# Performance work log

Measured on AMD Instinct MI355X. Metric: run time of the kernel, lower is better.

## Reference

```python
import jax, jax.numpy as jnp
import numpy as np

DIM = 192
NUM_HEADS = 8
EPS = 1e-12  # torch F.normalize default eps


def setup_inputs() -> dict:
    key = jax.random.key(0)
    k1, k2, k3, k4 = jax.random.split(key, 4)
    b, c, h, w = 8, DIM, 128, 128
    x = jax.random.normal(k1, (b, c, h, w), dtype=jnp.float32)
    # 1x1 qkv conv weight, stored as (3c, c)
    w_qkv = jax.random.normal(k2, (3 * c, c), dtype=jnp.float32) * (1.0 / np.sqrt(c))
    # depthwise 3x3 conv weight, groups = 3c -> OIHW (3c, 1, 3, 3)
    w_dw = jax.random.normal(k3, (3 * c, 1, 3, 3), dtype=jnp.float32) * (1.0 / 3.0)
    # 1x1 project_out weight (c, c)
    w_out = jax.random.normal(k4, (c, c), dtype=jnp.float32) * (1.0 / np.sqrt(c))
    temperature = jnp.ones((NUM_HEADS, 1, 1), dtype=jnp.float32)
    return {"x": x, "w_qkv": w_qkv, "w_dw": w_dw, "w_out": w_out,
            "temperature": temperature}


def _mdta(x, w_qkv, w_dw, w_out, temperature):
    b, c, h, w = x.shape
    nh = NUM_HEADS
    # 1x1 conv == channel GEMM
    qkv = jnp.einsum('oc,bchw->bohw', w_qkv, x)
    # depthwise 3x3 conv, groups = 3c
    qkv = jax.lax.conv_general_dilated(
        qkv, w_dw, window_strides=(1, 1), padding='SAME',
        feature_group_count=3 * c,
        dimension_numbers=('NCHW', 'OIHW', 'NCHW'))
    q, k, v = jnp.split(qkv, 3, axis=1)
    hd = c // nh
    q = q.reshape(b, nh, hd, h * w)
    k = k.reshape(b, nh, hd, h * w)
    v = v.reshape(b, nh, hd, h * w)
    # L2 normalize over spatial (hw) dim
    q = q / jnp.maximum(jnp.linalg.norm(q, axis=-1, keepdims=True), EPS)
    k = k / jnp.maximum(jnp.linalg.norm(k, axis=-1, keepdims=True), EPS)
    # channel x channel attention per head: (b, nh, hd, hd)
    attn = jnp.einsum('bhcn,bhdn->bhcd', q, k) * temperature
    attn = jax.nn.softmax(attn, axis=-1)
    out = jnp.einsum('bhcd,bhdn->bhcn', attn, v).reshape(b, c, h, w)
    return jnp.einsum('oc,bchw->bohw', w_out, out)


def reference(x, w_qkv, w_dw, w_out, temperature):
    return _mdta(x, w_qkv, w_dw, w_out, temperature)
```

## Files before the change

### kernel.cpp

```cpp
#include <hip/hip_runtime.h>


#define HW 16384
#define WIMG 128
#define C 192
#define C3 576
#define NH 8
#define HD 24

typedef unsigned short ushort8_t __attribute__((ext_vector_type(8)));
typedef unsigned short ushort4_t __attribute__((ext_vector_type(4)));
typedef short short8_t __attribute__((ext_vector_type(8)));
typedef float float4_t __attribute__((ext_vector_type(4)));

__device__ __forceinline__ float bfu2f(unsigned short u) {
    union { unsigned int i; float f; } v; v.i = ((unsigned int)u) << 16; return v.f;
}
__device__ __forceinline__ unsigned short f2bfu(float f) {
    union { float f; unsigned int i; } v; v.f = f;
    unsigned int x = v.i;
    return (unsigned short)((x + 0x7FFFu + ((x >> 16) & 1u)) >> 16);
}
__device__ __forceinline__ float inload(const void* p, int idx, int isbf) {
    return isbf ? bfu2f(((const unsigned short*)p)[idx]) : ((const float*)p)[idx];
}

__global__ void probe_dtype(const unsigned int* __restrict__ x, int* __restrict__ flag) {
    const int t = threadIdx.x;
    int cnt = 0;
    for (int i = t; i < 512; i += 256) {
        const unsigned int u = x[i] & 0xFFFFu;
        const unsigned int e = (u >> 7) & 0xFFu;
        if (u == 0u || (e >= 100u && e <= 140u)) cnt++;
    }
#pragma unroll
    for (int off = 32; off; off >>= 1) cnt += __shfl_down(cnt, off, 64);
    __shared__ int s[4];
    if ((t & 63) == 0) s[t >> 6] = cnt;
    __syncthreads();
    if (t == 0) flag[0] = (s[0] + s[1] + s[2] + s[3] > 300) ? 1 : 0;
}

__global__ void prep(const void* __restrict__ wqkv, const void* __restrict__ wdw,
                     const void* __restrict__ wout, const void* __restrict__ temp,
                     const int* __restrict__ flagp, unsigned short* __restrict__ wqb,
                     float* __restrict__ wdwf, float* __restrict__ woutf,
                     float* __restrict__ tempf, float* __restrict__ Sraw,
                     float* __restrict__ normsum) {
    const int isbf = flagp[0];
    const int id = blockIdx.x * 256 + threadIdx.x;
    const int stride = gridDim.x * 256;
    for (int i = id; i < C3 * C; i += stride)
        wqb[i] = isbf ? ((const unsigned short*)wqkv)[i] : f2bfu(((const float*)wqkv)[i]);
    for (int i = id; i < C3 * 9; i += stride) wdwf[i] = inload(wdw, i, isbf);
    for (int i = id; i < C * C; i += stride) woutf[i] = inload(wout, i, isbf);
    for (int i = id; i < NH; i += stride) tempf[i] = inload(temp, i, isbf);
    for (int i = id; i < 8 * NH * HD * HD; i += stride) Sraw[i] = 0.f;
    for (int i = id; i < 8 * 2 * C; i += stride) normsum[i] = 0.f;
}

__global__ __launch_bounds__(512) void gemm_mfma(
    const void* __restrict__ Bsrc, const unsigned short* __restrict__ Abf,
    void* __restrict__ outp, const int* __restrict__ flagp,
    size_t b_batch_stride, size_t b_const_off, size_t o_batch_stride,
    int a_batch_stride, int m_tiles, int b_mode, int out_mode) {
    __shared__ unsigned short xT[24576];
    const int isbf = flagp[0];
    const int b_isbf = b_mode | isbf;
    const int tid = threadIdx.x;
    const int batch = blockIdx.y;
    const int n0 = blockIdx.x * 128;
    const size_t b_off = b_batch_stride * batch + b_const_off;
    const size_t o_off = o_batch_stride * batch;
    const unsigned short* Ab = Abf + (size_t)a_batch_stride * batch;

    if (tid < 384) {
        const int cg = tid >> 4;
        const int pg = tid & 15;
        ushort8_t rows[8];
        if (b_isbf) {
            const unsigned short* bp = (const unsigned short*)Bsrc + b_off + n0 + pg * 8;
#pragma unroll
            for (int r = 0; r < 8; r++)
                rows[r] = *reinterpret_cast<const ushort8_t*>(bp + (size_t)(cg * 8 + r) * HW);
        } else {
            const float* bp = (const float*)Bsrc + b_off + n0 + pg * 8;
#pragma unroll
            for (int r = 0; r < 8; r++) {
                const float4_t f0 = *reinterpret_cast<const float4_t*>(bp + (size_t)(cg * 8 + r) * HW);
                const float4_t f1 = *reinterpret_cast<const float4_t*>(bp + (size_t)(cg * 8 + r) * HW + 4);
#pragma unroll
                for (int i = 0; i < 4; i++) { rows[r][i] = f2bfu(f0[i]); rows[r][i + 4] = f2bfu(f1[i]); }
            }
        }
#pragma unroll
        for (int s = 0; s < 8; s++) {
            ushort8_t outv;
#pragma unroll
            for (int r = 0; r < 8; r++) outv[r] = rows[r][s];
            const int p = pg * 8 + s;
            const int cidx = p * 24 + (cg ^ (p & 7));
            *reinterpret_cast<ushort8_t*>(&xT[cidx * 8]) = outv;
        }
    }

    const int w = tid >> 6;
    const int lane = tid & 63;
    const int l15 = lane & 15;
    const int quad = lane >> 4;
    const int mhalf = w & 1;
    const int nquad = w >> 1;

    __syncthreads();

    short8_t bfr[6][2];
#pragma unroll
    for (int ks = 0; ks < 6; ks++)
#pragma unroll
        for (int nt = 0; nt < 2; nt++) {
            const int p = nquad * 32 + nt * 16 + l15;
            const int cg = ks * 4 + quad;
            const int cidx = p * 24 + (cg ^ (p & 7));
            bfr[ks][nt] = *reinterpret_cast<const short8_t*>(&xT[cidx * 8]);
        }

    const int o_isbf = out_mode ? isbf : 1;
    for (int mt0 = 0; mt0 < m_tiles; mt0++) {
        const int m0 = mt0 * 64;
        short8_t afr[2][6];
#pragma unroll
        for (int mt = 0; mt < 2; mt++) {
            const int row = m0 + (mhalf * 2 + mt) * 16 + l15;
#pragma unroll
            for (int ks = 0; ks < 6; ks++)
                afr[mt][ks] = *reinterpret_cast<const short8_t*>(Ab + (size_t)row * C + ks * 32 + quad * 8);
        }
        float4_t acc[2][2];
#pragma unroll
        for (int mt = 0; mt < 2; mt++)
#pragma unroll
            for (int nt = 0; nt < 2; nt++) {
                float4_t z = {0.f, 0.f, 0.f, 0.f};
                acc[mt][nt] = z;
            }
#pragma unroll
        for (int ks = 0; ks < 6; ks++)
#pragma unroll
            for (int mt = 0; mt < 2; mt++)
#pragma unroll
                for (int nt = 0; nt < 2; nt++)
                    acc[mt][nt] = __builtin_amdgcn_mfma_f32_16x16x32_bf16(
                        afr[mt][ks], bfr[ks][nt], acc[mt][nt], 0, 0, 0);
#pragma unroll
        for (int mt = 0; mt < 2; mt++) {
            const int row = m0 + (mhalf * 2 + mt) * 16 + quad * 4;
#pragma unroll
            for (int nt = 0; nt < 2; nt++) {
                const int col = n0 + nquad * 32 + nt * 16 + l15;
#pragma unroll
                for (int r = 0; r < 4; r++) {
                    const size_t idx = o_off + (size_t)(row + r) * HW + col;
                    if (o_isbf) ((unsigned short*)outp)[idx] = f2bfu(acc[mt][nt][r]);
                    else ((float*)outp)[idx] = acc[mt][nt][r];
                }
            }
        }
    }
}

__global__ void dwconv(const unsigned short* __restrict__ qkv0,
                       const float* __restrict__ wdwf,
                       unsigned short* __restrict__ qkv1,
                       float* __restrict__ normsum) {
    const int ch = blockIdx.y;
    const size_t base = (size_t)blockIdx.z * C3 * HW + (size_t)ch * HW;
    const unsigned short* ip = qkv0 + base;
    const float* wp = wdwf + ch * 9;
    const int p = blockIdx.x * 2048 + threadIdx.x * 8;
    const int y = p >> 7, x0 = p & 127;
    float acc[8];
#pragma unroll
    for (int j = 0; j < 8; j++) acc[j] = 0.f;
#pragma unroll
    for (int dy = 0; dy < 3; dy++) {
        const int yy = y + dy - 1;
        if (yy < 0 || yy > 127) continue;
        const int rb = yy * WIMG + x0;
        const ushort8_t mid = *reinterpret_cast<const ushort8_t*>(ip + rb);
        float f[10];
        f[0] = (x0 > 0) ? bfu2f(ip[rb - 1]) : 0.f;
        f[9] = (x0 < 120) ? bfu2f(ip[rb + 8]) : 0.f;
#pragma unroll
        for (int i = 0; i < 8; i++) f[i + 1] = bfu2f(mid[i]);
        const float w0 = wp[dy * 3], w1 = wp[dy * 3 + 1], w2 = wp[dy * 3 + 2];
#pragma unroll
        for (int j = 0; j < 8; j++) acc[j] += w0 * f[j] + w1 * f[j + 1] + w2 * f[j + 2];
    }
    ushort8_t outv;
#pragma unroll
    for (int j = 0; j < 8; j++) outv[j] = f2bfu(acc[j]);
    *reinterpret_cast<ushort8_t*>(qkv1 + base + p) = outv;

    if (ch < 2 * C) {
        float ss = 0.f;
#pragma unroll
        for (int j = 0; j < 8; j++) ss += acc[j] * acc[j];
#pragma unroll
        for (int off = 32; off; off >>= 1) ss += __shfl_down(ss, off, 64);
        __shared__ float red[4];
        if ((threadIdx.x & 63) == 0) red[threadIdx.x >> 6] = ss;
        __syncthreads();
        if (threadIdx.x == 0)
            atomicAdd(&normsum[blockIdx.z * 2 * C + ch],
                      red[0] + red[1] + red[2] + red[3]);
    }
}

__global__ __launch_bounds__(256) void attn_gram(
    const unsigned short* __restrict__ qkv1, float* __restrict__ Sraw) {
    const int b = blockIdx.z, h = blockIdx.y;
    const int wave = threadIdx.x >> 6;
    const int lane = threadIdx.x & 63;
    const int l15 = lane & 15, quad = lane >> 4;
    const int k0 = (blockIdx.x * 4 + wave) * 512;
    const unsigned short* qrow = qkv1 + (size_t)b * C3 * HW + (size_t)(h * HD) * HW;
    const unsigned short* krow = qkv1 + (size_t)b * C3 * HW + (size_t)(C + h * HD) * HW;

    float4_t acc[2][2];
#pragma unroll
    for (int mt = 0; mt < 2; mt++)
#pragma unroll
        for (int nt = 0; nt < 2; nt++) {
            float4_t z = {0.f, 0.f, 0.f, 0.f};
            acc[mt][nt] = z;
        }

#pragma unroll 4
    for (int ks = 0; ks < 16; ks++) {
        const int kk = k0 + ks * 32 + quad * 8;
        short8_t qa[2], kb[2];
        qa[0] = *reinterpret_cast<const short8_t*>(qrow + (size_t)l15 * HW + kk);
        qa[1] = *reinterpret_cast<const short8_t*>(qrow + (size_t)(16 + l15) * HW + kk);
        kb[0] = *reinterpret_cast<const short8_t*>(krow + (size_t)l15 * HW + kk);
        kb[1] = *reinterpret_cast<const short8_t*>(krow + (size_t)(16 + l15) * HW + kk);
#pragma unroll
        for (int mt = 0; mt < 2; mt++)
#pragma unroll
            for (int nt = 0; nt < 2; nt++)
                acc[mt][nt] = __builtin_amdgcn_mfma_f32_16x16x32_bf16(
                    qa[mt], kb[nt], acc[mt][nt], 0, 0, 0);
    }

    float* Sb = Sraw + (size_t)b * NH * HD * HD + (size_t)h * HD * HD;
#pragma unroll
    for (int nt = 0; nt < 2; nt++) {
        const int j = nt * 16 + l15;
        if (j >= HD) continue;
#pragma unroll
        for (int mt = 0; mt < 2; mt++) {
            const int i0 = mt * 16 + quad * 4;
#pragma unroll
            for (int r = 0; r < 4; r++) {
                const int i = i0 + r;
                if (i < HD) atomicAdd(&Sb[i * HD + j], acc[mt][nt][r]);
            }
        }
    }
}

__global__ void buildM(const float* __restrict__ Sraw, const float* __restrict__ normsum,
                       const float* __restrict__ tempf, const float* __restrict__ woutf,
                       unsigned short* __restrict__ Mb) {
    __shared__ float As[NH * HD * HD];
    __shared__ float inv[2 * C];
    const int b = blockIdx.y;
    const int tid = threadIdx.x;
    for (int r = tid; r < 2 * C; r += 256)
        inv[r] = 1.f / fmaxf(sqrtf(normsum[b * 2 * C + r]), 1e-12f);
    __syncthreads();
    for (int e = tid; e < NH * HD * HD; e += 256) {
        const int h = e / (HD * HD);
        const int rm = e - h * HD * HD;
        const int i = rm / HD, j = rm % HD;
        As[e] = Sraw[(size_t)b * NH * HD * HD + e] * inv[h * HD + i] * inv[C + h * HD + j] * tempf[h];
    }
    __syncthreads();
    if (tid < C) {
        const int h = tid / HD, i = tid % HD;
        float* rp = As + h * HD * HD + i * HD;
        float mx = -1e30f;
#pragma unroll
        for (int j = 0; j < HD; j++) mx = fmaxf(mx, rp[j]);
        float sum = 0.f;
#pragma unroll
        for (int j = 0; j < HD; j++) { rp[j] = __expf(rp[j] - mx); sum += rp[j]; }
        const float is = 1.f / sum;
#pragma unroll
        for (int j = 0; j < HD; j++) rp[j] *= is;
    }
    __syncthreads();
    const int idx = blockIdx.x * 256 + tid;
    const int o = idx / C, dg = idx % C;
    const int h = dg / HD, d = dg % HD;
    const float* wp = woutf + o * C + h * HD;
    const float* Ap = As + h * HD * HD + d;
    float acc = 0.f;
#pragma unroll
    for (int c2 = 0; c2 < HD; c2++) acc += wp[c2] * Ap[c2 * HD];
    Mb[(size_t)b * C * C + o * C + dg] = f2bfu(acc);
}

extern "C" void kernel_launch(void* const* d_in, const int* in_sizes, int n_in,
                              void* d_out, int out_size, void* d_ws, size_t ws_size,
                              hipStream_t stream) {
    const void* x    = d_in[0];
    const void* wqkv = d_in[1];
    const void* wdw  = d_in[2];
    const void* wout = d_in[3];
    const void* temp = d_in[4];

    char* w = (char*)d_ws;
    int* flag = (int*)w;                          w += 64;
    unsigned short* wqb = (unsigned short*)w;     w += (size_t)C3 * C * 2;
    unsigned short* Mb  = (unsigned short*)w;     w += (size_t)8 * C * C * 2;
    float* wdwf  = (float*)w;                     w += (size_t)C3 * 9 * 4;
    float* woutf = (float*)w;                     w += (size_t)C * C * 4;
    float* tempf = (float*)w;                     w += 64;
    float* normsum = (float*)w;                   w += (size_t)8 * 2 * C * 4;
    float* Sraw  = (float*)w;                     w += (size_t)8 * NH * HD * HD * 4;
    unsigned short* qkv0 = (unsigned short*)w;    w += (size_t)8 * C3 * HW * 2;
    unsigned short* qkv1 = (unsigned short*)w;

    probe_dtype<<<1, 256, 0, stream>>>((const unsigned int*)x, flag);
    prep<<<432, 256, 0, stream>>>(wqkv, wdw, wout, temp, flag, wqb, wdwf, woutf,
                                  tempf, Sraw, normsum);
    gemm_mfma<<<dim3(HW / 128, 8), 512, 0, stream>>>(
        x, wqb, qkv0, flag, (size_t)C * HW, 0, (size_t)C3 * HW, 0, 9, 0, 0);
    dwconv<<<dim3(8, C3, 8), 256, 0, stream>>>(qkv0, wdwf, qkv1, normsum);
    attn_gram<<<dim3(8, NH, 8), 256, 0, stream>>>(qkv1, Sraw);
    buildM<<<dim3(144, 8), 256, 0, stream>>>(Sraw, normsum, tempf, woutf, Mb);
    gemm_mfma<<<dim3(HW / 128, 8), 512, 0, stream>>>(
        qkv1, Mb, d_out, flag, (size_t)C3 * HW, (size_t)2 * C * HW, (size_t)C * HW,
        C * C, 3, 1, 1);
}
```

Baseline: 456.6 us.

## Prepack GEMM A-operand in MFMA fragment order and stage bf16 output through LDS

Weights (qkv and per-batch fused M) are written in MFMA A-fragment order so each lane's A load becomes one contiguous 16-byte read. The B staging buffer is cut from 48KB to 32KB by loading the 192 channels in two halves with an extra barrier, which may raise occupancy. bf16 outputs are transposed through LDS so each thread writes 16-element contiguous rows instead of scattered 2-byte stores. This adds extra barriers per m-tile and reuses the LDS buffer.

```diff
diff --git a/kernel.cpp b/kernel.cpp
--- a/kernel.cpp
+++ b/kernel.cpp
@@ -9,7 +9,6 @@
 #define HD 24
 
 typedef unsigned short ushort8_t __attribute__((ext_vector_type(8)));
-typedef unsigned short ushort4_t __attribute__((ext_vector_type(4)));
 typedef short short8_t __attribute__((ext_vector_type(8)));
 typedef float float4_t __attribute__((ext_vector_type(4)));
 
@@ -23,6 +22,11 @@
 }
 __device__ __forceinline__ float inload(const void* p, int idx, int isbf) {
     return isbf ? bfu2f(((const unsigned short*)p)[idx]) : ((const float*)p)[idx];
+}
+
+__device__ __forceinline__ int afrag_idx(int o, int dg) {
+    return ((((o >> 4) * 6 + (dg >> 5)) * 4 + ((dg >> 3) & 3)) << 7)
+           + ((o & 15) << 3) + (dg & 7);
 }
 
 __global__ void probe_dtype(const unsigned int* __restrict__ x, int* __restrict__ flag) {
@@ -50,8 +54,12 @@
     const int isbf = flagp[0];
     const int id = blockIdx.x * 256 + threadIdx.x;
     const int stride = gridDim.x * 256;
-    for (int i = id; i < C3 * C; i += stride)
-        wqb[i] = isbf ? ((const unsigned short*)wqkv)[i] : f2bfu(((const float*)wqkv)[i]);
+    for (int i = id; i < C3 * C; i += stride) {
+        const int o = i / C, dg = i - o * C;
+        const unsigned short v =
+            isbf ? ((const unsigned short*)wqkv)[i] : f2bfu(((const float*)wqkv)[i]);
+        wqb[afrag_idx(o, dg)] = v;
+    }
     for (int i = id; i < C3 * 9; i += stride) wdwf[i] = inload(wdw, i, isbf);
     for (int i = id; i < C * C; i += stride) woutf[i] = inload(wout, i, isbf);
     for (int i = id; i < NH; i += stride) tempf[i] = inload(temp, i, isbf);
@@ -64,7 +72,7 @@
     void* __restrict__ outp, const int* __restrict__ flagp,
     size_t b_batch_stride, size_t b_const_off, size_t o_batch_stride,
     int a_batch_stride, int m_tiles, int b_mode, int out_mode) {
-    __shared__ unsigned short xT[24576];
+    __shared__ unsigned short sbuf[16384];
     const int isbf = flagp[0];
     const int b_isbf = b_mode | isbf;
     const int tid = threadIdx.x;
@@ -74,36 +82,6 @@
     const size_t o_off = o_batch_stride * batch;
     const unsigned short* Ab = Abf + (size_t)a_batch_stride * batch;
 
-    if (tid < 384) {
-        const int cg = tid >> 4;
-        const int pg = tid & 15;
-        ushort8_t rows[8];
-        if (b_isbf) {
-            const unsigned short* bp = (const unsigned short*)Bsrc + b_off + n0 + pg * 8;
-#pragma unroll
-            for (int r = 0; r < 8; r++)
-                rows[r] = *reinterpret_cast<const ushort8_t*>(bp + (size_t)(cg * 8 + r) * HW);
-        } else {
-            const float* bp = (const float*)Bsrc + b_off + n0 + pg * 8;
-#pragma unroll
-            for (int r = 0; r < 8; r++) {
-                const float4_t f0 = *reinterpret_cast<const float4_t*>(bp + (size_t)(cg * 8 + r) * HW);
-                const float4_t f1 = *reinterpret_cast<const float4_t*>(bp + (size_t)(cg * 8 + r) * HW + 4);
-#pragma unroll
-                for (int i = 0; i < 4; i++) { rows[r][i] = f2bfu(f0[i]); rows[r][i + 4] = f2bfu(f1[i]); }
-            }
-        }
-#pragma unroll
-        for (int s = 0; s < 8; s++) {
-            ushort8_t outv;
-#pragma unroll
-            for (int r = 0; r < 8; r++) outv[r] = rows[r][s];
-            const int p = pg * 8 + s;
-            const int cidx = p * 24 + (cg ^ (p & 7));
-            *reinterpret_cast<ushort8_t*>(&xT[cidx * 8]) = outv;
-        }
-    }
-
     const int w = tid >> 6;
     const int lane = tid & 63;
     const int l15 = lane & 15;
@@ -111,29 +89,67 @@
     const int mhalf = w & 1;
     const int nquad = w >> 1;
 
-    __syncthreads();
-
     short8_t bfr[6][2];
 #pragma unroll
-    for (int ks = 0; ks < 6; ks++)
-#pragma unroll
-        for (int nt = 0; nt < 2; nt++) {
-            const int p = nquad * 32 + nt * 16 + l15;
-            const int cg = ks * 4 + quad;
-            const int cidx = p * 24 + (cg ^ (p & 7));
-            bfr[ks][nt] = *reinterpret_cast<const short8_t*>(&xT[cidx * 8]);
-        }
+    for (int h = 0; h < 2; h++) {
+        if (h) __syncthreads();
+        if (tid < 192) {
+            const int cg = tid >> 4;
+            const int pg = tid & 15;
+            const int chbase = h * 96 + cg * 8;
+            ushort8_t rows[8];
+            if (b_isbf) {
+                const unsigned short* bp = (const unsigned short*)Bsrc + b_off + n0 + pg * 8;
+#pragma unroll
+                for (int r = 0; r < 8; r++)
+                    rows[r] = *reinterpret_cast<const ushort8_t*>(bp + (size_t)(chbase + r) * HW);
+            } else {
+                const float* bp = (const float*)Bsrc + b_off + n0 + pg * 8;
+#pragma unroll
+                for (int r = 0; r < 8; r++) {
+                    const float4_t f0 = *reinterpret_cast<const float4_t*>(bp + (size_t)(chbase + r) * HW);
+                    const float4_t f1 = *reinterpret_cast<const float4_t*>(bp + (size_t)(chbase + r) * HW + 4);
+#pragma unroll
+                    for (int i = 0; i < 4; i++) { rows[r][i] = f2bfu(f0[i]); rows[r][i + 4] = f2bfu(f1[i]); }
+                }
+            }
+#pragma unroll
+            for (int s = 0; s < 8; s++) {
+                ushort8_t outv;
+#pragma unroll
+                for (int r = 0; r < 8; r++) outv[r] = rows[r][s];
+                const int p = pg * 8 + s;
+                const int cidx = p * 16 + (cg ^ s);
+                *reinterpret_cast<ushort8_t*>(&sbuf[cidx * 8]) = outv;
+            }
+        }
+        __syncthreads();
+#pragma unroll
+        for (int ksl = 0; ksl < 3; ksl++) {
+            const int ks = h * 3 + ksl;
+            const int cgl = ks * 4 + quad - h * 12;
+#pragma unroll
+            for (int nt = 0; nt < 2; nt++) {
+                const int p = nquad * 32 + nt * 16 + l15;
+                const int cidx = p * 16 + (cgl ^ (p & 7));
+                bfr[ks][nt] = *reinterpret_cast<const short8_t*>(&sbuf[cidx * 8]);
+            }
+        }
+    }
 
     const int o_isbf = out_mode ? isbf : 1;
+    const int rr = tid >> 3;
+    const int kk = tid & 7;
     for (int mt0 = 0; mt0 < m_tiles; mt0++) {
         const int m0 = mt0 * 64;
         short8_t afr[2][6];
 #pragma unroll
         for (int mt = 0; mt < 2; mt++) {
-            const int row = m0 + (mhalf * 2 + mt) * 16 + l15;
+            const int tile = mt0 * 4 + mhalf * 2 + mt;
 #pragma unroll
             for (int ks = 0; ks < 6; ks++)
-                afr[mt][ks] = *reinterpret_cast<const short8_t*>(Ab + (size_t)row * C + ks * 32 + quad * 8);
+                afr[mt][ks] = *reinterpret_cast<const short8_t*>(
+                    Ab + (size_t)((((tile * 6 + ks) << 2) + quad) << 7) + (l15 << 3));
         }
         float4_t acc[2][2];
 #pragma unroll
@@ -151,17 +167,35 @@
                 for (int nt = 0; nt < 2; nt++)
                     acc[mt][nt] = __builtin_amdgcn_mfma_f32_16x16x32_bf16(
                         afr[mt][ks], bfr[ks][nt], acc[mt][nt], 0, 0, 0);
-#pragma unroll
-        for (int mt = 0; mt < 2; mt++) {
-            const int row = m0 + (mhalf * 2 + mt) * 16 + quad * 4;
-#pragma unroll
-            for (int nt = 0; nt < 2; nt++) {
-                const int col = n0 + nquad * 32 + nt * 16 + l15;
-#pragma unroll
-                for (int r = 0; r < 4; r++) {
-                    const size_t idx = o_off + (size_t)(row + r) * HW + col;
-                    if (o_isbf) ((unsigned short*)outp)[idx] = f2bfu(acc[mt][nt][r]);
-                    else ((float*)outp)[idx] = acc[mt][nt][r];
+        if (o_isbf) {
+            __syncthreads();
+#pragma unroll
+            for (int mt = 0; mt < 2; mt++) {
+                const int row64 = (mhalf * 2 + mt) * 16 + quad * 4;
+#pragma unroll
+                for (int nt = 0; nt < 2; nt++) {
+                    const int col = nquad * 32 + nt * 16 + l15;
+#pragma unroll
+                    for (int r = 0; r < 4; r++)
+                        sbuf[(row64 + r) * 136 + col] = f2bfu(acc[mt][nt][r]);
+                }
+            }
+            __syncthreads();
+            const ushort8_t v0 = *reinterpret_cast<const ushort8_t*>(&sbuf[rr * 136 + kk * 16]);
+            const ushort8_t v1 = *reinterpret_cast<const ushort8_t*>(&sbuf[rr * 136 + kk * 16 + 8]);
+            unsigned short* op = (unsigned short*)outp + o_off + (size_t)(m0 + rr) * HW + n0 + kk * 16;
+            *reinterpret_cast<ushort8_t*>(op) = v0;
+            *reinterpret_cast<ushort8_t*>(op + 8) = v1;
+        } else {
+#pragma unroll
+            for (int mt = 0; mt < 2; mt++) {
+                const int row = m0 + (mhalf * 2 + mt) * 16 + quad * 4;
+#pragma unroll
+                for (int nt = 0; nt < 2; nt++) {
+                    const int col = n0 + nquad * 32 + nt * 16 + l15;
+#pragma unroll
+                    for (int r = 0; r < 4; r++)
+                        ((float*)outp)[o_off + (size_t)(row + r) * HW + col] = acc[mt][nt][r];
                 }
             }
         }
@@ -307,7 +341,7 @@
     float acc = 0.f;
 #pragma unroll
     for (int c2 = 0; c2 < HD; c2++) acc += wp[c2] * Ap[c2 * HD];
-    Mb[(size_t)b * C * C + o * C + dg] = f2bfu(acc);
+    Mb[(size_t)b * C * C + afrag_idx(o, dg)] = f2bfu(acc);
 }
 
 extern "C" void kernel_launch(void* const* d_in, const int* in_sizes, int n_in,
```

Result: faster. 382.0 us (-16.4%).
